# Kernel optimization log

Measured on AMD Instinct MI355X. Metric: run time of the kernel, lower is better.

Reference implementation:

```python
import jax, jax.numpy as jnp
import numpy as np

B, L, D, H = 1, 4096, 768, 12
HD = D // H  # 64
NEG_INF = jnp.finfo(jnp.float32).min


def rmsnorm(x, g, eps=1e-6):
    return x * jax.lax.rsqrt(jnp.mean(x * x, axis=-1, keepdims=True) + eps) * g


def activation_quant(x):
    # per-token 8-bit fake quant
    scale = 127.0 / jnp.clip(jnp.max(jnp.abs(x), axis=-1, keepdims=True), 1e-5)
    return jnp.clip(jnp.round(x * scale), -128, 127) / scale


def weight_quant(w):
    # per-tensor 1.58-bit (ternary) fake quant
    scale = 1.0 / jnp.clip(jnp.mean(jnp.abs(w)), 1e-5)
    return jnp.clip(jnp.round(w * scale), -1, 1) / scale


def bitlinear(x, w, g):
    xn = rmsnorm(x, g)
    xq = xn + jax.lax.stop_gradient(activation_quant(xn) - xn)  # STE
    wq = w + jax.lax.stop_gradient(weight_quant(w) - w)          # STE
    return xq @ wq.T


def rope(x, cos, sin):
    # x: [B,L,H,HD]; cos/sin: [L,HD/2] -> broadcast [1,L,1,HD/2]
    xr = x.reshape(*x.shape[:-1], HD // 2, 2)
    x0, x1 = xr[..., 0], xr[..., 1]
    c = cos[None, :, None, :]
    s = sin[None, :, None, :]
    o0 = x0 * c - x1 * s
    o1 = x0 * s + x1 * c
    return jnp.stack([o0, o1], axis=-1).reshape(x.shape)


def setup_inputs() -> dict:
    key = jax.random.key(0)
    k1, k2, k3 = jax.random.split(key, 3)
    hidden_states = jax.random.normal(k1, (B, L, D), dtype=jnp.float32)
    mask = jnp.ones((B, L), dtype=bool)
    # standard RoPE angles, theta=10000
    freqs = 1.0 / (10000.0 ** (np.arange(0, HD, 2, dtype=np.float32) / HD))
    ang = np.outer(np.arange(L, dtype=np.float32), freqs)
    rot_cos = jnp.asarray(np.cos(ang), dtype=jnp.float32)
    rot_sin = jnp.asarray(np.sin(ang), dtype=jnp.float32)
    w_qkv = jax.random.truncated_normal(k2, -2.0, 2.0, (3 * D, D), dtype=jnp.float32) * 0.002
    w_o = jax.random.truncated_normal(k3, -2.0, 2.0, (D, D), dtype=jnp.float32) * 0.002
    g_qkv_norm = jnp.ones((D,), dtype=jnp.float32)
    g_o_norm = jnp.ones((D,), dtype=jnp.float32)
    return {"hidden_states": hidden_states, "mask": mask, "rot_cos": rot_cos,
            "rot_sin": rot_sin, "w_qkv": w_qkv, "w_o": w_o,
            "g_qkv_norm": g_qkv_norm, "g_o_norm": g_o_norm}


def reference(hidden_states, mask, rot_cos, rot_sin, w_qkv, w_o, g_qkv_norm, g_o_norm):
    qkv = bitlinear(hidden_states, w_qkv, g_qkv_norm)        # [B,L,3D]
    xq, xk, xv = jnp.split(qkv, 3, axis=-1)
    xq = xq.reshape(B, L, H, HD)
    xk = xk.reshape(B, L, H, HD)
    xv = xv.reshape(B, L, H, HD)
    xq = rope(xq, rot_cos, rot_sin)
    xk = rope(xk, rot_cos, rot_sin)
    scale = 1.0 / jnp.sqrt(jnp.float32(HD))
    scores = jnp.einsum('blhd,bmhd->bhlm', xq, xk) * scale   # [B,H,L,L]
    bias = jnp.where(mask[:, None, :, None], 0.0, NEG_INF)   # [B,1,L,1]
    attn = jax.nn.softmax(scores + bias, axis=-1)
    out = jnp.einsum('bhlm,bmhd->blhd', attn, xv).reshape(B, L, D)
    return bitlinear(out, w_o, g_o_norm)                      # dropout_p = 0.0
```

## Files before the change

kernel.cpp:

```cpp
#include <hip/hip_runtime.h>
#include <hip/hip_bf16.h>
#include <cstdint>
#include <cstddef>

typedef __attribute__((ext_vector_type(8))) short short8;
typedef __attribute__((ext_vector_type(4))) float f32x4;
typedef unsigned short u16;
typedef unsigned int u32;

#define DEV __device__ __forceinline__

DEV float bf2f(u16 u){ union{unsigned int i; float f;} v; v.i=((unsigned int)u)<<16; return v.f; }
DEV u16 f2bf(float x){ union{float f; unsigned int i;} v; v.f=x; unsigned int b=v.i; return (u16)((b + 0x7FFFu + ((b>>16)&1u))>>16); }
DEV u32 packbf2(float lo, float hi){
  __hip_bfloat162 h2 = __float22bfloat162_rn(float2{lo, hi});
  union{ __hip_bfloat162 h; u32 u; } cv; cv.h = h2; return cv.u;
}
DEV void gll16(const void* gsrc, void* lds){
  __builtin_amdgcn_global_load_lds((const __attribute__((address_space(1))) unsigned int*)gsrc,
                                   (__attribute__((address_space(3))) unsigned int*)lds, 16, 0, 0);
}

__global__ __launch_bounds__(256) void prelude(
    const float* __restrict__ wa, int na, const float* __restrict__ wb, int nb,
    float* __restrict__ pa, float* __restrict__ pb,
    const float* __restrict__ x, const float* __restrict__ g,
    u16* __restrict__ xq, float* __restrict__ deq)
{
  if(blockIdx.x < 512){
    __shared__ float red[256];
    const bool second = blockIdx.x >= 256;
    const float4* w4 = (const float4*)(second ? wb : wa);
    const int n4     = (second ? nb : na) >> 2;
    float* part      = second ? pb : pa;
    const int b0     = second ? (int)blockIdx.x - 256 : (int)blockIdx.x;
    float s=0.f;
    for(int i=b0*256+threadIdx.x; i<n4; i+=256*256){
      float4 v = w4[i];
      s += (fabsf(v.x)+fabsf(v.y)) + (fabsf(v.z)+fabsf(v.w));
    }
    red[threadIdx.x]=s; __syncthreads();
    for(int st=128; st>0; st>>=1){ if(threadIdx.x<st) red[threadIdx.x]+=red[threadIdx.x+st]; __syncthreads(); }
    if(threadIdx.x==0) part[b0]=red[0];
  } else {
    const int t = threadIdx.x, lane = t&63, w = t>>6;
    const int row = ((int)blockIdx.x - 512)*4 + w;
    const float* xr = x + (size_t)row*768;
    float4 v[3], gg[3];
#pragma unroll
    for(int j=0;j<3;j++){
      v[j]  = *(const float4*)(xr + lane*4 + j*256);
      gg[j] = *(const float4*)(g  + lane*4 + j*256);
    }
    float ss = 0.f;
#pragma unroll
    for(int j=0;j<3;j++) ss += v[j].x*v[j].x + v[j].y*v[j].y + v[j].z*v[j].z + v[j].w*v[j].w;
#pragma unroll
    for(int d=1; d<64; d<<=1) ss += __shfl_xor(ss, d, 64);
    float rn = rsqrtf(ss*(1.0f/768.f) + 1e-6f);
    float n[12];
#pragma unroll
    for(int j=0;j<3;j++){
      n[j*4+0]=v[j].x*rn*gg[j].x; n[j*4+1]=v[j].y*rn*gg[j].y;
      n[j*4+2]=v[j].z*rn*gg[j].z; n[j*4+3]=v[j].w*rn*gg[j].w;
    }
    float am = 0.f;
#pragma unroll
    for(int e=0;e<12;e++) am = fmaxf(am, fabsf(n[e]));
#pragma unroll
    for(int d=1; d<64; d<<=1) am = fmaxf(am, __shfl_xor(am, d, 64));
    float mx = fmaxf(am, 1e-5f);
    float sc = 127.f/mx;
    u16* o = xq + (size_t)row*768;
#pragma unroll
    for(int j=0;j<3;j++){
      u16 tmp[4];
#pragma unroll
      for(int e=0;e<4;e++){
        float q = fminf(127.f, fmaxf(-128.f, rintf(n[j*4+e]*sc)));
        tmp[e] = f2bf(q);
      }
      *(uint2*)(o + lane*4 + j*256) = *(uint2*)tmp;
    }
    if(lane==0) deq[row]=mx*(1.0f/127.f);
  }
}

__global__ void quant_weight2(const float* __restrict__ wa, int na, const float* __restrict__ pa_, float inva, float* __restrict__ sa, u16* __restrict__ qa,
                              const float* __restrict__ wb, int nb, const float* __restrict__ pb_, float invb, float* __restrict__ sb, u16* __restrict__ qb){
  __shared__ float red[256];
  const bool second = blockIdx.x >= 1024;
  const float* part = second ? pb_ : pa_;
  red[threadIdx.x] = part[threadIdx.x]; __syncthreads();
  for(int st=128; st>0; st>>=1){ if(threadIdx.x<st) red[threadIdx.x]+=red[threadIdx.x+st]; __syncthreads(); }
  float scale = fmaxf(red[0]*(second?invb:inva), 1e-5f);
  const float4* w4 = (const float4*)(second ? wb : wa);
  u16* q           = second ? qb : qa;
  const int n4     = (second ? nb : na) >> 2;
  const int b0     = second ? (int)blockIdx.x - 1024 : (int)blockIdx.x;
  const int nblk   = second ? 512 : 1024;
  if(threadIdx.x==0 && b0==0) (second?sb:sa)[0] = scale;
  float inv = 1.0f/scale;
  for(int i=b0*256+threadIdx.x; i<n4; i+=nblk*256){
    float4 v = w4[i];
    u16 tmp[4];
    tmp[0]=f2bf(fminf(1.f,fmaxf(-1.f,rintf(v.x*inv))));
    tmp[1]=f2bf(fminf(1.f,fmaxf(-1.f,rintf(v.y*inv))));
    tmp[2]=f2bf(fminf(1.f,fmaxf(-1.f,rintf(v.z*inv))));
    tmp[3]=f2bf(fminf(1.f,fmaxf(-1.f,rintf(v.w*inv))));
    *(uint2*)(q + (size_t)i*4) = *(uint2*)tmp;
  }
}

__global__ __launch_bounds__(256) void rms_quant(const float* __restrict__ x, const float* __restrict__ g,
                          u16* __restrict__ xq, float* __restrict__ deq){
  const int t = threadIdx.x, lane = t&63, w = t>>6;
  const int row = blockIdx.x*4 + w;
  const float* xr = x + (size_t)row*768;
  float4 v[3], gg[3];
#pragma unroll
  for(int j=0;j<3;j++){
    v[j]  = *(const float4*)(xr + lane*4 + j*256);
    gg[j] = *(const float4*)(g  + lane*4 + j*256);
  }
  float ss = 0.f;
#pragma unroll
  for(int j=0;j<3;j++) ss += v[j].x*v[j].x + v[j].y*v[j].y + v[j].z*v[j].z + v[j].w*v[j].w;
#pragma unroll
  for(int d=1; d<64; d<<=1) ss += __shfl_xor(ss, d, 64);
  float rn = rsqrtf(ss*(1.0f/768.f) + 1e-6f);
  float n[12];
#pragma unroll
  for(int j=0;j<3;j++){
    n[j*4+0]=v[j].x*rn*gg[j].x; n[j*4+1]=v[j].y*rn*gg[j].y;
    n[j*4+2]=v[j].z*rn*gg[j].z; n[j*4+3]=v[j].w*rn*gg[j].w;
  }
  float am = 0.f;
#pragma unroll
  for(int e=0;e<12;e++) am = fmaxf(am, fabsf(n[e]));
#pragma unroll
  for(int d=1; d<64; d<<=1) am = fmaxf(am, __shfl_xor(am, d, 64));
  float mx = fmaxf(am, 1e-5f);
  float sc = 127.f/mx;
  u16* o = xq + (size_t)row*768;
#pragma unroll
  for(int j=0;j<3;j++){
    u16 tmp[4];
#pragma unroll
    for(int e=0;e<4;e++){
      float q = fminf(127.f, fmaxf(-128.f, rintf(n[j*4+e]*sc)));
      tmp[e] = f2bf(q);
    }
    *(uint2*)(o + lane*4 + j*256) = *(uint2*)tmp;
  }
  if(lane==0) deq[row]=mx*(1.0f/127.f);
}

template<int BM, int BN>
__global__ __launch_bounds__(256) void gemm_bt(
    const u16* __restrict__ A, const u16* __restrict__ B,
    int M, int N, int K,
    const float* __restrict__ rdeq, const float* __restrict__ wsc,
    u16* __restrict__ Cb, float* __restrict__ Cf)
{
  constexpr int MR = BM/32, NR = BN/32;
  constexpr int SA = BM/64, SB = BN/64;
  __shared__ u16 lA[3][4][BM][8];
  __shared__ u16 lB[3][4][BN][8];
  const int t = threadIdx.x, lane = t&63, w = t>>6;
  const int wr = (w>>1)*(BM/2), wc = (w&1)*(BN/2);
  const int rowBase = blockIdx.y*BM, colBase = blockIdx.x*BN;
  const int g = lane>>4, lr = lane&15;
  f32x4 acc[MR][NR];
#pragma unroll
  for(int m=0;m<MR;m++)
#pragma unroll
    for(int n=0;n<NR;n++) acc[m][n]={0.f,0.f,0.f,0.f};

  auto stage = [&](int p, int k0){
#pragma unroll
    for(int i=0;i<SA;i++){
      int s = t + i*256, r = s & (BM-1), kg = s / BM;
      gll16(A + (size_t)(rowBase+r)*K + k0 + kg*8, &lA[p][kg][r][0]);
    }
#pragma unroll
    for(int i=0;i<SB;i++){
      int s = t + i*256, r = s & (BN-1), kg = s / BN;
      gll16(B + (size_t)(colBase+r)*K + k0 + kg*8, &lB[p][kg][r][0]);
    }
  };

  const int nk = K>>5;
  stage(0, 0);
  if(nk>1) stage(1, 32);
  int p = 0;
  for(int kt=0; kt<nk; ++kt){
    if(kt+2<nk) stage((p+2)%3, (kt+2)<<5);
    if constexpr (SA+SB == 4){
      if(kt+2<nk)      asm volatile("s_waitcnt vmcnt(8)" ::: "memory");
      else if(kt+1<nk) asm volatile("s_waitcnt vmcnt(4)" ::: "memory");
      else             asm volatile("s_waitcnt vmcnt(0)" ::: "memory");
    } else {
      if(kt+2<nk)      asm volatile("s_waitcnt vmcnt(4)" ::: "memory");
      else if(kt+1<nk) asm volatile("s_waitcnt vmcnt(2)" ::: "memory");
      else             asm volatile("s_waitcnt vmcnt(0)" ::: "memory");
    }
    __builtin_amdgcn_s_barrier();
    __builtin_amdgcn_sched_barrier(0);
    short8 af[MR], bfr[NR];
#pragma unroll
    for(int m=0;m<MR;m++) af[m]  = *(const short8*)&lA[p][g][wr + m*16 + lr][0];
#pragma unroll
    for(int n=0;n<NR;n++) bfr[n] = *(const short8*)&lB[p][g][wc + n*16 + lr][0];
#pragma unroll
    for(int m=0;m<MR;m++)
#pragma unroll
      for(int n=0;n<NR;n++)
        acc[m][n] = __builtin_amdgcn_mfma_f32_16x16x32_bf16(af[m], bfr[n], acc[m][n], 0,0,0);
    __builtin_amdgcn_s_barrier();
    p = (p+1)%3;
  }
  float ws = wsc[0];
#pragma unroll
  for(int m=0;m<MR;m++){
#pragma unroll
    for(int rr=0;rr<4;rr++){
      int row = rowBase + wr + m*16 + g*4 + rr;
      float rs = rdeq[row]*ws;
#pragma unroll
      for(int n=0;n<NR;n++){
        int col = colBase + wc + n*16 + lr;
        float v = acc[m][n][rr]*rs;
        if(Cb) Cb[(size_t)row*N+col]=f2bf(v);
        else   Cf[(size_t)row*N+col]=v;
      }
    }
  }
}

__global__ __launch_bounds__(256) void rope_split(const u16* __restrict__ qkv,
                           const float* __restrict__ cosb, const float* __restrict__ sinb,
                           u16* __restrict__ Qb, u16* __restrict__ Kb, u16* __restrict__ Vt)
{
  const int h = blockIdx.y, p0 = blockIdx.x*64, t = threadIdx.x;
#pragma unroll
  for(int it=0; it<8; ++it){
    int idx = it*256 + t;
    int pos = p0 + (idx>>5), j = idx&31;
    const u16* base = qkv + (size_t)pos*2304 + h*64;
    float q0=bf2f(base[2*j]), q1=bf2f(base[2*j+1]);
    float k0=bf2f(base[768+2*j]), k1=bf2f(base[768+2*j+1]);
    float c=cosb[pos*32+j], s=sinb[pos*32+j];
    size_t ob = ((size_t)h*4096 + pos)*64 + 2*j;
    Qb[ob]   = f2bf(q0*c - q1*s);
    Qb[ob+1] = f2bf(q0*s + q1*c);
    Kb[ob]   = f2bf(k0*c - k1*s);
    Kb[ob+1] = f2bf(k0*s + k1*c);
  }
  __shared__ u16 vt[64][72];
#pragma unroll
  for(int it=0; it<2; ++it){
    int idx = it*256 + t;
    int pos = idx>>3, db = idx&7;
    uint4 v = *(const uint4*)(qkv + (size_t)(p0+pos)*2304 + h*64 + 1536 + db*8);
    const u16* pv = (const u16*)&v;
#pragma unroll
    for(int e=0;e<8;e++) vt[db*8+e][pos] = pv[e];
  }
  __syncthreads();
#pragma unroll
  for(int it=0; it<2; ++it){
    int idx = it*256 + t;
    int d = idx>>3, pc = idx&7;
    uint4 tmp; u16* tp=(u16*)&tmp;
#pragma unroll
    for(int e=0;e<8;e++) tp[e]=vt[d][pc*8+e];
    *(uint4*)(Vt + ((size_t)h*64 + d)*4096 + p0 + pc*8) = tmp;
  }
}

__global__ __launch_bounds__(256) void attn(
    const u16* __restrict__ Qb, const u16* __restrict__ Kb,
    const u16* __restrict__ Vt, float* __restrict__ O)
{
  __shared__ u16 lK[8][128][8];
  __shared__ u16 lV[16][64][8];
  __shared__ u32 lPT[4][16][64];

  const int bid = blockIdx.x;
  const int swz = (bid&7)*96 + (bid>>3);
  const int h = swz>>6, q0 = (swz&63)*64;
  const int t = threadIdx.x, lane = t&63, w = t>>6;
  const int g = lane>>4, lr = lane&15;
  const int key = (lr<<2)&28;

  const float C = 0.125f*1.44269504088896f;
  const float thrRaw = 8.0f / C;

  short8 qf0, qf1;
  {
    const u16* qp = Qb + ((size_t)h*4096 + q0 + w*16 + lr)*64 + g*8;
    qf0 = *(const short8*)qp;
    qf1 = *(const short8*)(qp+32);
  }
  f32x4 o[4];
#pragma unroll
  for(int n=0;n<4;n++) o[n]={0.f,0.f,0.f,0.f};
  float m_run = -1e30f, l_run = 0.f;

  const u16* kb_lane = Kb + ((size_t)h*4096 + lane)*64;
  const u16* vb_lane = Vt + ((size_t)h*64  + lane)*4096;
  const int kvhalf = (w&1)*64;

  for(int it=0; it<32; ++it){
    const int kvb = it<<7;
    __syncthreads();
#pragma unroll
    for(int j=0;j<4;j++){
      int sl = j*4 + w;
      gll16(kb_lane + (size_t)(kvb + kvhalf)*64 + (sl>>1)*8, &lK[sl>>1][kvhalf][0]);
    }
#pragma unroll
    for(int j=0;j<4;j++){
      int sl = j*4 + w;
      gll16(vb_lane + kvb + sl*8, &lV[sl][0][0]);
    }
    __syncthreads();

    f32x4 s[8];
    __builtin_amdgcn_s_setprio(1);
#pragma unroll
    for(int nt=0;nt<8;nt++){
      f32x4 z = {0.f,0.f,0.f,0.f};
      short8 kf0 = *(const short8*)&lK[g  ][nt*16+lr][0];
      short8 kf1 = *(const short8*)&lK[g+4][nt*16+lr][0];
      z = __builtin_amdgcn_mfma_f32_16x16x32_bf16(kf0, qf0, z, 0,0,0);
      s[nt] = __builtin_amdgcn_mfma_f32_16x16x32_bf16(kf1, qf1, z, 0,0,0);
    }
    __builtin_amdgcn_s_setprio(0);

    f32x4 m4a = __builtin_elementwise_max(s[0], s[1]);
    f32x4 m4b = __builtin_elementwise_max(s[2], s[3]);
    f32x4 m4c = __builtin_elementwise_max(s[4], s[5]);
    f32x4 m4d = __builtin_elementwise_max(s[6], s[7]);
    f32x4 m4 = __builtin_elementwise_max(__builtin_elementwise_max(m4a, m4b),
                                         __builtin_elementwise_max(m4c, m4d));
    float mt = fmaxf(fmaxf(m4[0],m4[1]), fmaxf(m4[2],m4[3]));
    mt = fmaxf(mt, __shfl_xor(mt, 16, 64));
    mt = fmaxf(mt, __shfl_xor(mt, 32, 64));

    if(!__all(mt <= m_run + thrRaw)){
      float m_new = fmaxf(m_run, mt);
      float al = __builtin_amdgcn_exp2f((m_run - m_new)*C);
      m_run = m_new;
      l_run *= al;
      float alr[4];
#pragma unroll
      for(int r=0;r<4;r++) alr[r] = __shfl(al, g*4+r, 64);
#pragma unroll
      for(int nt=0;nt<4;nt++)
#pragma unroll
        for(int r=0;r<4;r++) o[nt][r]*=alr[r];
    }
    float mc = m_run * C;
    float ps = 0.f;
#pragma unroll
    for(int nt=0;nt<8;nt++){
      float p0 = __builtin_amdgcn_exp2f(__builtin_fmaf(s[nt][0], C, -mc));
      float p1 = __builtin_amdgcn_exp2f(__builtin_fmaf(s[nt][1], C, -mc));
      float p2 = __builtin_amdgcn_exp2f(__builtin_fmaf(s[nt][2], C, -mc));
      float p3 = __builtin_amdgcn_exp2f(__builtin_fmaf(s[nt][3], C, -mc));
      ps += (p0+p1)+(p2+p3);
      uint2 pk; pk.x = packbf2(p0,p1); pk.y = packbf2(p2,p3);
      *(uint2*)&lPT[w][lr][(nt*8 + g*2) ^ key] = pk;
    }
    l_run += ps;

#pragma unroll
    for(int c=0;c<4;c++){
      short8 pa = *(const short8*)&lPT[w][lr][(c*16 + g*4) ^ key];
#pragma unroll
      for(int nt=0;nt<4;nt++){
        short8 vf = *(const short8*)&lV[c*4+g][nt*16+lr][0];
        o[nt] = __builtin_amdgcn_mfma_f32_16x16x32_bf16(pa, vf, o[nt], 0,0,0);
      }
    }
  }
  l_run += __shfl_xor(l_run, 16, 64);
  l_run += __shfl_xor(l_run, 32, 64);
  float linv[4];
#pragma unroll
  for(int r=0;r<4;r++) linv[r] = 1.0f/__shfl(l_run, g*4+r, 64);
#pragma unroll
  for(int nt=0;nt<4;nt++)
#pragma unroll
    for(int r=0;r<4;r++){
      int row = q0 + w*16 + g*4 + r;
      O[(size_t)row*768 + h*64 + nt*16 + lr] = o[nt][r]*linv[r];
    }
}

extern "C" void kernel_launch(void* const* d_in, const int* in_sizes, int n_in,
                              void* d_out, int out_size, void* d_ws, size_t ws_size,
                              hipStream_t stream) {
  const float* hidden = (const float*)d_in[0];
  (void)d_in[1];
  const float* cosb = (const float*)d_in[2];
  const float* sinb = (const float*)d_in[3];
  const float* w_qkv = (const float*)d_in[4];
  const float* w_o   = (const float*)d_in[5];
  const float* g_qkv = (const float*)d_in[6];
  const float* g_o   = (const float*)d_in[7];
  float* out = (float*)d_out;
  (void)in_sizes; (void)n_in; (void)out_size;

  uint8_t* ws = (uint8_t*)d_ws;
  size_t off = 0;
  auto alloc = [&](size_t bytes)->size_t{ size_t o=off; off=(off+bytes+255)&~(size_t)255; return o; };
  size_t o_sc0  = alloc(4);
  size_t o_sc1  = alloc(4);
  size_t o_pt0  = alloc(256*4);
  size_t o_pt1  = alloc(256*4);
  size_t o_adeq = alloc(4096*4);
  size_t o_odeq = alloc(4096*4);
  size_t o_wq   = alloc((size_t)2304*768*2);
  size_t o_wo   = alloc((size_t)768*768*2);
  size_t o_xq   = alloc((size_t)4096*768*2);
  size_t o_qkv  = alloc((size_t)4096*2304*2);
  size_t o_q    = alloc((size_t)12*4096*64*2);
  size_t o_k    = alloc((size_t)12*4096*64*2);
  size_t o_vt   = alloc((size_t)12*64*4096*2);
  size_t o_of   = alloc((size_t)4096*768*4);
  size_t o_oq   = alloc((size_t)4096*768*2);
  if (off > ws_size) {
    hipMemsetAsync(d_out, 0, (size_t)out_size*4, stream);
    return;
  }
  float* sc0 = (float*)(ws+o_sc0); float* sc1 = (float*)(ws+o_sc1);
  float* pt0 = (float*)(ws+o_pt0); float* pt1 = (float*)(ws+o_pt1);
  float* adeq= (float*)(ws+o_adeq); float* odeq=(float*)(ws+o_odeq);
  u16* Wq  = (u16*)(ws+o_wq);  u16* Wo  = (u16*)(ws+o_wo);
  u16* Xq  = (u16*)(ws+o_xq);  u16* QKV = (u16*)(ws+o_qkv);
  u16* Qb  = (u16*)(ws+o_q);   u16* Kb  = (u16*)(ws+o_k);
  u16* Vt  = (u16*)(ws+o_vt);
  float* Of = (float*)(ws+o_of); u16* Oq = (u16*)(ws+o_oq);

  prelude<<<1536,256,0,stream>>>(w_qkv, 2304*768, w_o, 768*768, pt0, pt1,
                                 hidden, g_qkv, Xq, adeq);
  quant_weight2<<<1536,256,0,stream>>>(w_qkv, 2304*768, pt0, 1.0f/(2304.f*768.f), sc0, Wq,
                                       w_o,   768*768,  pt1, 1.0f/(768.f*768.f),  sc1, Wo);
  gemm_bt<128,128><<<dim3(18,32),256,0,stream>>>(Xq, Wq, 4096,2304,768, adeq, sc0, QKV, nullptr);
  rope_split<<<dim3(64,12),256,0,stream>>>(QKV, cosb, sinb, Qb, Kb, Vt);
  attn<<<768,256,0,stream>>>(Qb, Kb, Vt, Of);
  rms_quant<<<1024,256,0,stream>>>(Of, g_o, Oq, odeq);
  gemm_bt<64,64><<<dim3(12,64),256,0,stream>>>(Oq, Wo, 4096,768,768, odeq, sc1, nullptr, out);
}
```

Measured before the change: 191.5 us.

## Switch quantized activations and ternary weights to int8 with i8 MFMA GEMMs

Quantized activations and ternary weights are now stored as int8 instead of bf16, and both projection GEMMs use the 16x16x64 int8 MFMA with int32 accumulation. This halves the bytes moved for the quantized operands and doubles K per MFMA, so there are half as many K iterations. The results stay exact because the values are small integers, but the GEMMs are only part of the total, and attention probably dominates the runtime.

```diff
diff --git a/kernel.cpp b/kernel.cpp
--- a/kernel.cpp
+++ b/kernel.cpp
@@ -5,8 +5,10 @@
 
 typedef __attribute__((ext_vector_type(8))) short short8;
 typedef __attribute__((ext_vector_type(4))) float f32x4;
+typedef __attribute__((ext_vector_type(4))) int i32x4;
 typedef unsigned short u16;
 typedef unsigned int u32;
+typedef signed char i8s;
 
 #define DEV __device__ __forceinline__
 
@@ -16,6 +18,10 @@
   __hip_bfloat162 h2 = __float22bfloat162_rn(float2{lo, hi});
   union{ __hip_bfloat162 h; u32 u; } cv; cv.h = h2; return cv.u;
 }
+DEV u32 pack4i8(float a, float b, float c, float d){
+  int ia=(int)a, ib=(int)b, ic=(int)c, id=(int)d;
+  return (u32)(ia & 0xff) | (((u32)(ib & 0xff))<<8) | (((u32)(ic & 0xff))<<16) | (((u32)(id & 0xff))<<24);
+}
 DEV void gll16(const void* gsrc, void* lds){
   __builtin_amdgcn_global_load_lds((const __attribute__((address_space(1))) unsigned int*)gsrc,
                                    (__attribute__((address_space(3))) unsigned int*)lds, 16, 0, 0);
@@ -25,7 +31,7 @@
     const float* __restrict__ wa, int na, const float* __restrict__ wb, int nb,
     float* __restrict__ pa, float* __restrict__ pb,
     const float* __restrict__ x, const float* __restrict__ g,
-    u16* __restrict__ xq, float* __restrict__ deq)
+    i8s* __restrict__ xq, float* __restrict__ deq)
 {
   if(blockIdx.x < 512){
     __shared__ float red[256];
@@ -71,23 +77,21 @@
     for(int d=1; d<64; d<<=1) am = fmaxf(am, __shfl_xor(am, d, 64));
     float mx = fmaxf(am, 1e-5f);
     float sc = 127.f/mx;
-    u16* o = xq + (size_t)row*768;
+    i8s* o = xq + (size_t)row*768;
 #pragma unroll
     for(int j=0;j<3;j++){
-      u16 tmp[4];
-#pragma unroll
-      for(int e=0;e<4;e++){
-        float q = fminf(127.f, fmaxf(-128.f, rintf(n[j*4+e]*sc)));
-        tmp[e] = f2bf(q);
-      }
-      *(uint2*)(o + lane*4 + j*256) = *(uint2*)tmp;
+      float q0 = fminf(127.f, fmaxf(-128.f, rintf(n[j*4+0]*sc)));
+      float q1 = fminf(127.f, fmaxf(-128.f, rintf(n[j*4+1]*sc)));
+      float q2 = fminf(127.f, fmaxf(-128.f, rintf(n[j*4+2]*sc)));
+      float q3 = fminf(127.f, fmaxf(-128.f, rintf(n[j*4+3]*sc)));
+      *(u32*)(o + lane*4 + j*256) = pack4i8(q0,q1,q2,q3);
     }
     if(lane==0) deq[row]=mx*(1.0f/127.f);
   }
 }
 
-__global__ void quant_weight2(const float* __restrict__ wa, int na, const float* __restrict__ pa_, float inva, float* __restrict__ sa, u16* __restrict__ qa,
-                              const float* __restrict__ wb, int nb, const float* __restrict__ pb_, float invb, float* __restrict__ sb, u16* __restrict__ qb){
+__global__ void quant_weight2(const float* __restrict__ wa, int na, const float* __restrict__ pa_, float inva, float* __restrict__ sa, i8s* __restrict__ qa,
+                              const float* __restrict__ wb, int nb, const float* __restrict__ pb_, float invb, float* __restrict__ sb, i8s* __restrict__ qb){
   __shared__ float red[256];
   const bool second = blockIdx.x >= 1024;
   const float* part = second ? pb_ : pa_;
@@ -95,7 +99,7 @@
   for(int st=128; st>0; st>>=1){ if(threadIdx.x<st) red[threadIdx.x]+=red[threadIdx.x+st]; __syncthreads(); }
   float scale = fmaxf(red[0]*(second?invb:inva), 1e-5f);
   const float4* w4 = (const float4*)(second ? wb : wa);
-  u16* q           = second ? qb : qa;
+  i8s* q           = second ? qb : qa;
   const int n4     = (second ? nb : na) >> 2;
   const int b0     = second ? (int)blockIdx.x - 1024 : (int)blockIdx.x;
   const int nblk   = second ? 512 : 1024;
@@ -103,17 +107,16 @@
   float inv = 1.0f/scale;
   for(int i=b0*256+threadIdx.x; i<n4; i+=nblk*256){
     float4 v = w4[i];
-    u16 tmp[4];
-    tmp[0]=f2bf(fminf(1.f,fmaxf(-1.f,rintf(v.x*inv))));
-    tmp[1]=f2bf(fminf(1.f,fmaxf(-1.f,rintf(v.y*inv))));
-    tmp[2]=f2bf(fminf(1.f,fmaxf(-1.f,rintf(v.z*inv))));
-    tmp[3]=f2bf(fminf(1.f,fmaxf(-1.f,rintf(v.w*inv))));
-    *(uint2*)(q + (size_t)i*4) = *(uint2*)tmp;
+    float q0 = fminf(1.f,fmaxf(-1.f,rintf(v.x*inv)));
+    float q1 = fminf(1.f,fmaxf(-1.f,rintf(v.y*inv)));
+    float q2 = fminf(1.f,fmaxf(-1.f,rintf(v.z*inv)));
+    float q3 = fminf(1.f,fmaxf(-1.f,rintf(v.w*inv)));
+    *(u32*)(q + (size_t)i*4) = pack4i8(q0,q1,q2,q3);
   }
 }
 
 __global__ __launch_bounds__(256) void rms_quant(const float* __restrict__ x, const float* __restrict__ g,
-                          u16* __restrict__ xq, float* __restrict__ deq){
+                          i8s* __restrict__ xq, float* __restrict__ deq){
   const int t = threadIdx.x, lane = t&63, w = t>>6;
   const int row = blockIdx.x*4 + w;
   const float* xr = x + (size_t)row*768;
@@ -142,60 +145,58 @@
   for(int d=1; d<64; d<<=1) am = fmaxf(am, __shfl_xor(am, d, 64));
   float mx = fmaxf(am, 1e-5f);
   float sc = 127.f/mx;
-  u16* o = xq + (size_t)row*768;
+  i8s* o = xq + (size_t)row*768;
 #pragma unroll
   for(int j=0;j<3;j++){
-    u16 tmp[4];
-#pragma unroll
-    for(int e=0;e<4;e++){
-      float q = fminf(127.f, fmaxf(-128.f, rintf(n[j*4+e]*sc)));
-      tmp[e] = f2bf(q);
-    }
-    *(uint2*)(o + lane*4 + j*256) = *(uint2*)tmp;
+    float q0 = fminf(127.f, fmaxf(-128.f, rintf(n[j*4+0]*sc)));
+    float q1 = fminf(127.f, fmaxf(-128.f, rintf(n[j*4+1]*sc)));
+    float q2 = fminf(127.f, fmaxf(-128.f, rintf(n[j*4+2]*sc)));
+    float q3 = fminf(127.f, fmaxf(-128.f, rintf(n[j*4+3]*sc)));
+    *(u32*)(o + lane*4 + j*256) = pack4i8(q0,q1,q2,q3);
   }
   if(lane==0) deq[row]=mx*(1.0f/127.f);
 }
 
 template<int BM, int BN>
-__global__ __launch_bounds__(256) void gemm_bt(
-    const u16* __restrict__ A, const u16* __restrict__ B,
+__global__ __launch_bounds__(256) void gemm_i8(
+    const i8s* __restrict__ A, const i8s* __restrict__ B,
     int M, int N, int K,
     const float* __restrict__ rdeq, const float* __restrict__ wsc,
     u16* __restrict__ Cb, float* __restrict__ Cf)
 {
   constexpr int MR = BM/32, NR = BN/32;
   constexpr int SA = BM/64, SB = BN/64;
-  __shared__ u16 lA[3][4][BM][8];
-  __shared__ u16 lB[3][4][BN][8];
+  __shared__ i8s lA[3][4][BM][16];
+  __shared__ i8s lB[3][4][BN][16];
   const int t = threadIdx.x, lane = t&63, w = t>>6;
   const int wr = (w>>1)*(BM/2), wc = (w&1)*(BN/2);
   const int rowBase = blockIdx.y*BM, colBase = blockIdx.x*BN;
   const int g = lane>>4, lr = lane&15;
-  f32x4 acc[MR][NR];
+  i32x4 acc[MR][NR];
 #pragma unroll
   for(int m=0;m<MR;m++)
 #pragma unroll
-    for(int n=0;n<NR;n++) acc[m][n]={0.f,0.f,0.f,0.f};
+    for(int n=0;n<NR;n++) acc[m][n]={0,0,0,0};
 
   auto stage = [&](int p, int k0){
 #pragma unroll
     for(int i=0;i<SA;i++){
       int s = t + i*256, r = s & (BM-1), kg = s / BM;
-      gll16(A + (size_t)(rowBase+r)*K + k0 + kg*8, &lA[p][kg][r][0]);
+      gll16(A + (size_t)(rowBase+r)*K + k0 + kg*16, &lA[p][kg][r][0]);
     }
 #pragma unroll
     for(int i=0;i<SB;i++){
       int s = t + i*256, r = s & (BN-1), kg = s / BN;
-      gll16(B + (size_t)(colBase+r)*K + k0 + kg*8, &lB[p][kg][r][0]);
+      gll16(B + (size_t)(colBase+r)*K + k0 + kg*16, &lB[p][kg][r][0]);
     }
   };
 
-  const int nk = K>>5;
+  const int nk = K>>6;
   stage(0, 0);
-  if(nk>1) stage(1, 32);
+  if(nk>1) stage(1, 64);
   int p = 0;
   for(int kt=0; kt<nk; ++kt){
-    if(kt+2<nk) stage((p+2)%3, (kt+2)<<5);
+    if(kt+2<nk) stage((p+2)%3, (kt+2)<<6);
     if constexpr (SA+SB == 4){
       if(kt+2<nk)      asm volatile("s_waitcnt vmcnt(8)" ::: "memory");
       else if(kt+1<nk) asm volatile("s_waitcnt vmcnt(4)" ::: "memory");
@@ -207,16 +208,16 @@
     }
     __builtin_amdgcn_s_barrier();
     __builtin_amdgcn_sched_barrier(0);
-    short8 af[MR], bfr[NR];
-#pragma unroll
-    for(int m=0;m<MR;m++) af[m]  = *(const short8*)&lA[p][g][wr + m*16 + lr][0];
-#pragma unroll
-    for(int n=0;n<NR;n++) bfr[n] = *(const short8*)&lB[p][g][wc + n*16 + lr][0];
+    i32x4 af[MR], bfr[NR];
+#pragma unroll
+    for(int m=0;m<MR;m++) af[m]  = *(const i32x4*)&lA[p][g][wr + m*16 + lr][0];
+#pragma unroll
+    for(int n=0;n<NR;n++) bfr[n] = *(const i32x4*)&lB[p][g][wc + n*16 + lr][0];
 #pragma unroll
     for(int m=0;m<MR;m++)
 #pragma unroll
       for(int n=0;n<NR;n++)
-        acc[m][n] = __builtin_amdgcn_mfma_f32_16x16x32_bf16(af[m], bfr[n], acc[m][n], 0,0,0);
+        acc[m][n] = __builtin_amdgcn_mfma_i32_16x16x64_i8(af[m], bfr[n], acc[m][n], 0,0,0);
     __builtin_amdgcn_s_barrier();
     p = (p+1)%3;
   }
@@ -230,7 +231,7 @@
 #pragma unroll
       for(int n=0;n<NR;n++){
         int col = colBase + wc + n*16 + lr;
-        float v = acc[m][n][rr]*rs;
+        float v = (float)acc[m][n][rr]*rs;
         if(Cb) Cb[(size_t)row*N+col]=f2bf(v);
         else   Cf[(size_t)row*N+col]=v;
       }
@@ -423,15 +424,15 @@
   size_t o_pt1  = alloc(256*4);
   size_t o_adeq = alloc(4096*4);
   size_t o_odeq = alloc(4096*4);
-  size_t o_wq   = alloc((size_t)2304*768*2);
-  size_t o_wo   = alloc((size_t)768*768*2);
-  size_t o_xq   = alloc((size_t)4096*768*2);
+  size_t o_wq   = alloc((size_t)2304*768);
+  size_t o_wo   = alloc((size_t)768*768);
+  size_t o_xq   = alloc((size_t)4096*768);
   size_t o_qkv  = alloc((size_t)4096*2304*2);
   size_t o_q    = alloc((size_t)12*4096*64*2);
   size_t o_k    = alloc((size_t)12*4096*64*2);
   size_t o_vt   = alloc((size_t)12*64*4096*2);
   size_t o_of   = alloc((size_t)4096*768*4);
-  size_t o_oq   = alloc((size_t)4096*768*2);
+  size_t o_oq   = alloc((size_t)4096*768);
   if (off > ws_size) {
     hipMemsetAsync(d_out, 0, (size_t)out_size*4, stream);
     return;
@@ -439,19 +440,19 @@
   float* sc0 = (float*)(ws+o_sc0); float* sc1 = (float*)(ws+o_sc1);
   float* pt0 = (float*)(ws+o_pt0); float* pt1 = (float*)(ws+o_pt1);
   float* adeq= (float*)(ws+o_adeq); float* odeq=(float*)(ws+o_odeq);
-  u16* Wq  = (u16*)(ws+o_wq);  u16* Wo  = (u16*)(ws+o_wo);
-  u16* Xq  = (u16*)(ws+o_xq);  u16* QKV = (u16*)(ws+o_qkv);
+  i8s* Wq  = (i8s*)(ws+o_wq);  i8s* Wo  = (i8s*)(ws+o_wo);
+  i8s* Xq  = (i8s*)(ws+o_xq);  u16* QKV = (u16*)(ws+o_qkv);
   u16* Qb  = (u16*)(ws+o_q);   u16* Kb  = (u16*)(ws+o_k);
   u16* Vt  = (u16*)(ws+o_vt);
-  float* Of = (float*)(ws+o_of); u16* Oq = (u16*)(ws+o_oq);
+  float* Of = (float*)(ws+o_of); i8s* Oq = (i8s*)(ws+o_oq);
 
   prelude<<<1536,256,0,stream>>>(w_qkv, 2304*768, w_o, 768*768, pt0, pt1,
                                  hidden, g_qkv, Xq, adeq);
   quant_weight2<<<1536,256,0,stream>>>(w_qkv, 2304*768, pt0, 1.0f/(2304.f*768.f), sc0, Wq,
                                        w_o,   768*768,  pt1, 1.0f/(768.f*768.f),  sc1, Wo);
-  gemm_bt<128,128><<<dim3(18,32),256,0,stream>>>(Xq, Wq, 4096,2304,768, adeq, sc0, QKV, nullptr);
+  gemm_i8<128,128><<<dim3(18,32),256,0,stream>>>(Xq, Wq, 4096,2304,768, adeq, sc0, QKV, nullptr);
   rope_split<<<dim3(64,12),256,0,stream>>>(QKV, cosb, sinb, Qb, Kb, Vt);
   attn<<<768,256,0,stream>>>(Qb, Kb, Vt, Of);
   rms_quant<<<1024,256,0,stream>>>(Of, g_o, Oq, odeq);
-  gemm_bt<64,64><<<dim3(12,64),256,0,stream>>>(Oq, Wo, 4096,768,768, odeq, sc1, nullptr, out);
-}
+  gemm_i8<64,64><<<dim3(12,64),256,0,stream>>>(Oq, Wo, 4096,768,768, odeq, sc1, nullptr, out);
+}
```

After: 160.3 us. -16.3%, faster.
